# Optimization experiments

Measured on AMD Instinct MI355X. Metric: run time of the kernel, lower is better.

## Reference

```python
import jax, jax.numpy as jnp
import numpy as np

T, NUM_N, D = 4096, 16, 512


def setup_inputs() -> dict:
    key = jax.random.key(0)
    k1, k2, k3, k4 = jax.random.split(key, 4)
    x = jax.random.normal(k1, (T, D), dtype=jnp.float32)
    h_a = jax.random.normal(k2, (NUM_N, D), dtype=jnp.float32)
    h_s = jax.random.uniform(k3, (NUM_N, D), dtype=jnp.float32)      # init SD state (>=0)
    alpha = jax.random.uniform(k4, (NUM_N, D), dtype=jnp.float32)    # uniform(0,1) like init_N=None
    return {"x": x, "h_a": h_a, "h_s": h_s, "alpha": alpha}


def reference(x, h_a, h_s, alpha):
    # x: [T, D]; h_a, h_s, alpha: [N, D]
    h_v0 = h_s * h_s  # variance state

    def step(carry, x_i):
        ha, hv = carry
        d = x_i[None, :] - ha                       # [N, D]
        hv = (1.0 - alpha) * (hv + alpha * d * d)   # variance update (uses old ha)
        ha = alpha * d + ha                         # EMA update
        return (ha, hv), (ha, jnp.sqrt(hv))

    (ha_N, hv_N), (out_a, out_s) = jax.lax.scan(step, (h_a, h_v0), x)
    # out_a, out_s: [T, N, D]
    out = jnp.concatenate([out_a, out_s], axis=1)   # [T, 2N, D]
    return out, ha_N, jnp.sqrt(hv_N)
```

## Files before the change

kernel.cpp:

```cpp
#include <hip/hip_runtime.h>
#include <math.h>

#define T_  4096
#define D_  512
#define N_  16
#define S_  32
#define L_  128
#define ND_  (N_*D_)
#define SND_ (S_*ND_)

__global__ __launch_bounds__(256) void k1_seg_ha(const float* __restrict__ x,
                                                 const float* __restrict__ alpha,
                                                 float* __restrict__ P) {
    int gid = blockIdx.x * 256 + threadIdx.x;
    int d   = gid & (D_ - 1);
    int nd  = gid & (ND_ - 1);
    int s   = gid >> 13;
    float a  = alpha[nd];
    float ha = 0.0f;
    const float* xp = x + (size_t)s * L_ * D_ + d;
    #pragma unroll 4
    for (int t = 0; t < L_; ++t) {
        float xv = xp[(size_t)t * D_];
        ha = fmaf(a, xv - ha, ha);
    }
    P[gid] = ha;
}

__global__ __launch_bounds__(256) void k2_prefix_ha(const float* __restrict__ h_a,
                                                    const float* __restrict__ alpha,
                                                    const float* __restrict__ P,
                                                    float* __restrict__ haStart,
                                                    float* __restrict__ out_ha_final) {
    int nd = blockIdx.x * 256 + threadIdx.x;
    float a  = alpha[nd];
    float cL = powf(1.0f - a, (float)L_);
    float ha = h_a[nd];
    #pragma unroll
    for (int s = 0; s < S_; ++s) {
        haStart[s * ND_ + nd] = ha;
        ha = fmaf(cL, ha, P[s * ND_ + nd]);
    }
    out_ha_final[nd] = ha;
}

__global__ __launch_bounds__(256) void k3_seg_hv(const float* __restrict__ x,
                                                 const float* __restrict__ alpha,
                                                 const float* __restrict__ haStart,
                                                 float* __restrict__ Q) {
    int gid = blockIdx.x * 256 + threadIdx.x;
    int d   = gid & (D_ - 1);
    int nd  = gid & (ND_ - 1);
    int s   = gid >> 13;
    float a  = alpha[nd];
    float c  = 1.0f - a;
    float ha = haStart[gid];
    float hv = 0.0f;
    const float* xp = x + (size_t)s * L_ * D_ + d;
    #pragma unroll 2
    for (int t = 0; t < L_; ++t) {
        float xv = xp[(size_t)t * D_];
        float dd = xv - ha;
        hv = c * fmaf(a, dd * dd, hv);
        ha = fmaf(a, dd, ha);
    }
    Q[gid] = hv;
}

__global__ __launch_bounds__(256) void k4_prefix_hv(const float* __restrict__ h_s,
                                                    const float* __restrict__ alpha,
                                                    const float* __restrict__ Q,
                                                    float* __restrict__ hvStart,
                                                    float* __restrict__ out_hs_final) {
    int nd = blockIdx.x * 256 + threadIdx.x;
    float a  = alpha[nd];
    float cL = powf(1.0f - a, (float)L_);
    float hs = h_s[nd];
    float hv = hs * hs;
    #pragma unroll
    for (int s = 0; s < S_; ++s) {
        hvStart[s * ND_ + nd] = hv;
        hv = fmaf(cL, hv, Q[s * ND_ + nd]);
    }
    out_hs_final[nd] = sqrtf(hv);
}

__global__ __launch_bounds__(256) void k5_out(const float* __restrict__ x,
                                              const float* __restrict__ alpha,
                                              const float* __restrict__ haStart,
                                              const float* __restrict__ hvStart,
                                              float* __restrict__ out) {
    int gid = blockIdx.x * 256 + threadIdx.x;
    int d   = gid & (D_ - 1);
    int n   = (gid >> 9) & (N_ - 1);
    int nd  = gid & (ND_ - 1);
    int s   = gid >> 13;
    float a  = alpha[nd];
    float c  = 1.0f - a;
    float ha = haStart[gid];
    float hv = hvStart[gid];
    const float* xp = x + (size_t)s * L_ * D_ + d;
    float* oa = out + (size_t)s * L_ * 2 * ND_ + (size_t)n * D_ + d;
    float* os = oa + ND_;
    #pragma unroll 2
    for (int t = 0; t < L_; ++t) {
        float xv = xp[(size_t)t * D_];
        float dd = xv - ha;
        hv = c * fmaf(a, dd * dd, hv);
        ha = fmaf(a, dd, ha);
        oa[(size_t)t * 2 * ND_] = ha;
        os[(size_t)t * 2 * ND_] = sqrtf(hv);
    }
}

extern "C" void kernel_launch(void* const* d_in, const int* in_sizes, int n_in,
                              void* d_out, int out_size, void* d_ws, size_t ws_size,
                              hipStream_t stream) {
    const float* x     = (const float*)d_in[0];
    const float* h_a   = (const float*)d_in[1];
    const float* h_s   = (const float*)d_in[2];
    const float* alpha = (const float*)d_in[3];
    float* out = (float*)d_out;

    float* ws      = (float*)d_ws;
    float* P       = ws;
    float* haStart = ws + SND_;
    float* Q       = ws + 2 * (size_t)SND_;
    float* hvStart = ws + 3 * (size_t)SND_;

    float* out_ha_final = out + (size_t)T_ * 2 * ND_;
    float* out_hs_final = out_ha_final + ND_;

    dim3 b(256);
    dim3 segGrid(SND_ / 256);
    dim3 chGrid(ND_ / 256);

    k1_seg_ha<<<segGrid, b, 0, stream>>>(x, alpha, P);
    k2_prefix_ha<<<chGrid, b, 0, stream>>>(h_a, alpha, P, haStart, out_ha_final);
    k3_seg_hv<<<segGrid, b, 0, stream>>>(x, alpha, haStart, Q);
    k4_prefix_hv<<<chGrid, b, 0, stream>>>(h_s, alpha, Q, hvStart, out_hs_final);
    k5_out<<<segGrid, b, 0, stream>>>(x, alpha, haStart, hvStart, out);
}
```

Before: 312.6 us.

## Fuse EMA and variance segment scans via closed-form carry algebra

Each segment is now scanned once from a zero EMA start, recording the local EMA, the local variance and the sum of deviations. A single prefix kernel then combines both recurrences using a closed-form correction that depends on the incoming EMA. This cuts the pass count from five kernels to three, removing one full read of x and two workspace round-trips. It also swaps powf for repeated squaring, remaps block indices, and uses nontemporal stores plus a raw sqrt for the large output. The reassociated variance math may change rounding, and negative values are clamped to zero.

```diff
diff --git a/kernel.cpp b/kernel.cpp
--- a/kernel.cpp
+++ b/kernel.cpp
@@ -9,80 +9,76 @@
 #define ND_  (N_*D_)
 #define SND_ (S_*ND_)
 
-__global__ __launch_bounds__(256) void k1_seg_ha(const float* __restrict__ x,
-                                                 const float* __restrict__ alpha,
-                                                 float* __restrict__ P) {
-    int gid = blockIdx.x * 256 + threadIdx.x;
-    int d   = gid & (D_ - 1);
-    int nd  = gid & (ND_ - 1);
-    int s   = gid >> 13;
+__device__ __forceinline__ float pow_L(float c) {
+    float r = c * c;
+    r = r * r;
+    r = r * r;
+    r = r * r;
+    r = r * r;
+    r = r * r;
+    r = r * r;
+    return r;
+}
+
+__global__ __launch_bounds__(256) void k1_seg(const float* __restrict__ x,
+                                              const float* __restrict__ alpha,
+                                              float* __restrict__ P,
+                                              float* __restrict__ Q0,
+                                              float* __restrict__ S1) {
+    int bid  = blockIdx.x;
+    int obid = (bid & 7) * 128 + (bid >> 3);
+    int gid  = obid * 256 + threadIdx.x;
+    int d    = gid & (D_ - 1);
+    int nd   = gid & (ND_ - 1);
+    int s    = gid >> 13;
     float a  = alpha[nd];
-    float ha = 0.0f;
+    float c  = 1.0f - a;
+    float p = 0.0f, q = 0.0f, s1 = 0.0f;
     const float* xp = x + (size_t)s * L_ * D_ + d;
-    #pragma unroll 4
+    #pragma unroll 8
     for (int t = 0; t < L_; ++t) {
         float xv = xp[(size_t)t * D_];
-        ha = fmaf(a, xv - ha, ha);
+        float e  = xv - p;
+        q  = c * fmaf(a, e * e, q);
+        p  = fmaf(a, e, p);
+        s1 += e;
     }
-    P[gid] = ha;
+    P[gid]  = p;
+    Q0[gid] = q;
+    S1[gid] = s1;
 }
 
-__global__ __launch_bounds__(256) void k2_prefix_ha(const float* __restrict__ h_a,
-                                                    const float* __restrict__ alpha,
-                                                    const float* __restrict__ P,
-                                                    float* __restrict__ haStart,
-                                                    float* __restrict__ out_ha_final) {
-    int nd = blockIdx.x * 256 + threadIdx.x;
-    float a  = alpha[nd];
-    float cL = powf(1.0f - a, (float)L_);
-    float ha = h_a[nd];
-    #pragma unroll
-    for (int s = 0; s < S_; ++s) {
-        haStart[s * ND_ + nd] = ha;
-        ha = fmaf(cL, ha, P[s * ND_ + nd]);
-    }
-    out_ha_final[nd] = ha;
-}
-
-__global__ __launch_bounds__(256) void k3_seg_hv(const float* __restrict__ x,
+__global__ __launch_bounds__(256) void k2_prefix(const float* __restrict__ h_a,
+                                                 const float* __restrict__ h_s,
                                                  const float* __restrict__ alpha,
-                                                 const float* __restrict__ haStart,
-                                                 float* __restrict__ Q) {
-    int gid = blockIdx.x * 256 + threadIdx.x;
-    int d   = gid & (D_ - 1);
-    int nd  = gid & (ND_ - 1);
-    int s   = gid >> 13;
+                                                 float* __restrict__ P,
+                                                 float* __restrict__ Q0,
+                                                 const float* __restrict__ S1,
+                                                 float* __restrict__ out_ha_final,
+                                                 float* __restrict__ out_hs_final) {
+    int nd   = blockIdx.x * 256 + threadIdx.x;
     float a  = alpha[nd];
     float c  = 1.0f - a;
-    float ha = haStart[gid];
-    float hv = 0.0f;
-    const float* xp = x + (size_t)s * L_ * D_ + d;
-    #pragma unroll 2
-    for (int t = 0; t < L_; ++t) {
-        float xv = xp[(size_t)t * D_];
-        float dd = xv - ha;
-        hv = c * fmaf(a, dd * dd, hv);
-        ha = fmaf(a, dd, ha);
+    float cL = pow_L(c);
+    float k1 = 2.0f * a * cL;
+    float k2 = cL * (1.0f - cL);
+    float H  = h_a[nd];
+    float hs = h_s[nd];
+    float V  = hs * hs;
+    #pragma unroll 4
+    for (int s = 0; s < S_; ++s) {
+        size_t i = (size_t)s * ND_ + nd;
+        float p  = P[i];
+        float q  = Q0[i];
+        float s1 = S1[i];
+        P[i]  = H;
+        Q0[i] = V;
+        float Vn = cL * V + q - k1 * s1 * H + k2 * H * H;
+        V = fmaxf(Vn, 0.0f);
+        H = fmaf(cL, H, p);
     }
-    Q[gid] = hv;
-}
-
-__global__ __launch_bounds__(256) void k4_prefix_hv(const float* __restrict__ h_s,
-                                                    const float* __restrict__ alpha,
-                                                    const float* __restrict__ Q,
-                                                    float* __restrict__ hvStart,
-                                                    float* __restrict__ out_hs_final) {
-    int nd = blockIdx.x * 256 + threadIdx.x;
-    float a  = alpha[nd];
-    float cL = powf(1.0f - a, (float)L_);
-    float hs = h_s[nd];
-    float hv = hs * hs;
-    #pragma unroll
-    for (int s = 0; s < S_; ++s) {
-        hvStart[s * ND_ + nd] = hv;
-        hv = fmaf(cL, hv, Q[s * ND_ + nd]);
-    }
-    out_hs_final[nd] = sqrtf(hv);
+    out_ha_final[nd] = H;
+    out_hs_final[nd] = sqrtf(V);
 }
 
 __global__ __launch_bounds__(256) void k5_out(const float* __restrict__ x,
@@ -90,11 +86,13 @@
                                               const float* __restrict__ haStart,
                                               const float* __restrict__ hvStart,
                                               float* __restrict__ out) {
-    int gid = blockIdx.x * 256 + threadIdx.x;
-    int d   = gid & (D_ - 1);
-    int n   = (gid >> 9) & (N_ - 1);
-    int nd  = gid & (ND_ - 1);
-    int s   = gid >> 13;
+    int bid  = blockIdx.x;
+    int obid = (bid & 7) * 128 + (bid >> 3);
+    int gid  = obid * 256 + threadIdx.x;
+    int d    = gid & (D_ - 1);
+    int n    = (gid >> 9) & (N_ - 1);
+    int nd   = gid & (ND_ - 1);
+    int s    = gid >> 13;
     float a  = alpha[nd];
     float c  = 1.0f - a;
     float ha = haStart[gid];
@@ -102,14 +100,14 @@
     const float* xp = x + (size_t)s * L_ * D_ + d;
     float* oa = out + (size_t)s * L_ * 2 * ND_ + (size_t)n * D_ + d;
     float* os = oa + ND_;
-    #pragma unroll 2
+    #pragma unroll 4
     for (int t = 0; t < L_; ++t) {
         float xv = xp[(size_t)t * D_];
         float dd = xv - ha;
         hv = c * fmaf(a, dd * dd, hv);
         ha = fmaf(a, dd, ha);
-        oa[(size_t)t * 2 * ND_] = ha;
-        os[(size_t)t * 2 * ND_] = sqrtf(hv);
+        __builtin_nontemporal_store(ha, oa + (size_t)t * 2 * ND_);
+        __builtin_nontemporal_store(__builtin_amdgcn_sqrtf(hv), os + (size_t)t * 2 * ND_);
     }
 }
 
@@ -122,11 +120,10 @@
     const float* alpha = (const float*)d_in[3];
     float* out = (float*)d_out;
 
-    float* ws      = (float*)d_ws;
-    float* P       = ws;
-    float* haStart = ws + SND_;
-    float* Q       = ws + 2 * (size_t)SND_;
-    float* hvStart = ws + 3 * (size_t)SND_;
+    float* ws = (float*)d_ws;
+    float* P  = ws;
+    float* Q0 = ws + (size_t)SND_;
+    float* S1 = ws + 2 * (size_t)SND_;
 
     float* out_ha_final = out + (size_t)T_ * 2 * ND_;
     float* out_hs_final = out_ha_final + ND_;
@@ -135,9 +132,8 @@
     dim3 segGrid(SND_ / 256);
     dim3 chGrid(ND_ / 256);
 
-    k1_seg_ha<<<segGrid, b, 0, stream>>>(x, alpha, P);
-    k2_prefix_ha<<<chGrid, b, 0, stream>>>(h_a, alpha, P, haStart, out_ha_final);
-    k3_seg_hv<<<segGrid, b, 0, stream>>>(x, alpha, haStart, Q);
-    k4_prefix_hv<<<chGrid, b, 0, stream>>>(h_s, alpha, Q, hvStart, out_hs_final);
-    k5_out<<<segGrid, b, 0, stream>>>(x, alpha, haStart, hvStart, out);
+    k1_seg<<<segGrid, b, 0, stream>>>(x, alpha, P, Q0, S1);
+    k2_prefix<<<chGrid, b, 0, stream>>>(h_a, h_s, alpha, P, Q0, S1,
+                                        out_ha_final, out_hs_final);
+    k5_out<<<segGrid, b, 0, stream>>>(x, alpha, P, Q0, out);
 }
```

After: 296.6 us. 5.1% less time.
